# Performance work log

Hardware: AMD Instinct MI355X
Metric: run time of the kernel (lower is better)

## Reference

```python
import jax, jax.numpy as jnp
import numpy as np

NUM_UNITS = 64
NUM_NODES = 2048
COARSE_NODES = 256
INPUT_DIM = 1
BATCH = 64
AVG_DEGREE = 16


def _normalized_laplacian(adj):
    # A = A + I; L = D^-1/2 A^T D^-1/2 (matches scipy path in source)
    a = adj + np.eye(adj.shape[0], dtype=np.float64)
    d = a.sum(axis=1)
    d_inv_sqrt = np.power(d, -0.5)
    d_inv_sqrt[np.isinf(d_inv_sqrt)] = 0.0
    # (A @ D^-1/2).T @ D^-1/2 = A.T * d[:,None] * d[None,:]
    lap = a.T * d_inv_sqrt[:, None] * d_inv_sqrt[None, :]
    return lap.astype(np.float32)


def _random_adj(rng, n, deg):
    rows = np.repeat(np.arange(n), deg)
    cols = rng.integers(0, n, size=n * deg)
    a = np.zeros((n, n), dtype=np.float64)
    a[rows, cols] = 1.0
    a = np.maximum(a, a.T)  # symmetric
    np.fill_diagonal(a, 0.0)
    return a


def _xavier(key, shape):
    std = np.sqrt(2.0 / (shape[0] + shape[1]))
    return jax.random.normal(key, shape, dtype=jnp.float32) * std


def setup_inputs() -> dict:
    key = jax.random.key(0)
    ks = jax.random.split(key, 8)
    rng = np.random.default_rng(0)

    adj = jnp.asarray(_normalized_laplacian(_random_adj(rng, NUM_NODES, AVG_DEGREE)))
    adj1 = jnp.asarray(_normalized_laplacian(_random_adj(rng, COARSE_NODES, AVG_DEGREE)))
    # afc_mx in source is (num_nodes, coarse_nodes); afc = afc_mx.T, afct = afc_mx
    afc_mx = rng.random((NUM_NODES, COARSE_NODES)).astype(np.float32)
    afc = jnp.asarray(afc_mx.T)   # (C, N)
    afct = jnp.asarray(afc_mx)    # (N, C)

    in_size = INPUT_DIM + NUM_UNITS
    inputs = jax.random.normal(ks[0], (BATCH, NUM_NODES * INPUT_DIM), dtype=jnp.float32)
    state = jax.random.normal(ks[1], (BATCH, NUM_NODES * NUM_UNITS), dtype=jnp.float32)

    return {
        "inputs": inputs, "state": state,
        "adj": adj, "adj1": adj1, "afc": afc, "afct": afct,
        "w0": _xavier(ks[2], (in_size, 2 * NUM_UNITS)),
        "b0": jnp.zeros((2 * NUM_UNITS,), jnp.float32),
        "w1": _xavier(ks[3], (in_size, NUM_UNITS)),
        "b1": jnp.zeros((NUM_UNITS,), jnp.float32),
        "w01": _xavier(ks[4], (in_size, 2 * NUM_UNITS)),
        "b01": jnp.zeros((2 * NUM_UNITS,), jnp.float32),
        "w11": _xavier(ks[5], (in_size, NUM_UNITS)),
        "b11": jnp.zeros((NUM_UNITS,), jnp.float32),
    }


def _gc(inputs, state, adj, adj1, afc, afct, w, b, wf, bf):
    B = inputs.shape[0]
    N, C = adj.shape[0], adj1.shape[0]
    x = jnp.concatenate([inputs.reshape(B, N, -1), state.reshape(B, N, -1)], axis=2)
    F = x.shape[2]
    x0 = x.transpose(1, 2, 0).reshape(N, F * B)          # (N, F*B)
    x0fc = afc @ x0                                      # (C, F*B)
    x1 = adj @ x0                                        # graph conv, fine graph
    x1fc = adj1 @ x0fc                                   # graph conv, coarse graph
    x1 = x1 + jax.nn.sigmoid(afct @ x0fc)                # cross term fine<-coarse
    x1fc = x1fc + jax.nn.sigmoid(afc @ x1)               # cross term coarse<-fine
    out = x1.reshape(N, F, B).transpose(2, 0, 1).reshape(-1, F) @ w + b
    outfc = x1fc.reshape(C, F, B).transpose(2, 0, 1).reshape(-1, F) @ wf + bf
    return out.reshape(B, N, -1), outfc.reshape(B, C, -1)


def reference(inputs, state, adj, adj1, afc, afct, w0, b0, w1, b1, w01, b01, w11, b11):
    B = inputs.shape[0]
    N, U = NUM_NODES, NUM_UNITS
    x1, _x1fc = _gc(inputs, state, adj, adj1, afc, afct, w0, b0, w01, b01)
    value = jax.nn.sigmoid(x1)                           # (B, N, 2U)
    r, u = value[..., :U], value[..., U:]
    r = r.reshape(B, N * U)
    u = u.reshape(B, N * U)
    c0, _c1 = _gc(inputs, r * state, adj, adj1, afc, afct, w1, b1, w11, b11)
    c = jnp.tanh(c0).reshape(B, N * U)
    new_state = u * state + (1.0 - u) * c
    return new_state
```

## Files before the change

### kernel.cpp

```cpp
#include <hip/hip_runtime.h>
#include <hip/hip_bf16.h>
#include <math.h>

#define N_NODES 2048
#define C_NODES 256
#define BATCH   64
#define UNITS   64
#define JS      4096
#define NX      4160
#define JSX     4224
#define NU      131072
#define XSTR    4160
#define CAP     192

typedef short  s16x8 __attribute__((ext_vector_type(8)));
typedef float  f32x4 __attribute__((ext_vector_type(4)));

__device__ __forceinline__ float sigmoidf_(float x) { return 1.0f / (1.0f + __expf(-x)); }

__device__ __forceinline__ float bfs2f(short s) {
    union { float f; unsigned u; } w; w.u = ((unsigned)(unsigned short)s) << 16; return w.f;
}
__device__ __forceinline__ short f2bfs(float f) {
    __hip_bfloat16 h = __float2bfloat16(f);
    short s; __builtin_memcpy(&s, &h, 2); return s;
}

__device__ __forceinline__ void gload_lds16(const void* g, void* l) {
    __builtin_amdgcn_global_load_lds(
        (const __attribute__((address_space(1))) void*)g,
        (__attribute__((address_space(3))) void*)l, 16, 0, 0);
}

__global__ __launch_bounds__(256) void cvt_split(const float* __restrict__ s,
                                                 __hip_bfloat16* __restrict__ dh,
                                                 __hip_bfloat16* __restrict__ dl, int n)
{
    int stride = gridDim.x * 256;
    for (int i = blockIdx.x * 256 + threadIdx.x; i < n; i += stride) {
        float v = s[i];
        __hip_bfloat16 h = __float2bfloat16(v);
        dh[i] = h;
        dl[i] = __float2bfloat16(v - __bfloat162float(h));
    }
}

__global__ __launch_bounds__(256) void cvt_w(const float* __restrict__ w0,
                                             const float* __restrict__ w1,
                                             __hip_bfloat16* __restrict__ w0h, __hip_bfloat16* __restrict__ w0l,
                                             __hip_bfloat16* __restrict__ w1h, __hip_bfloat16* __restrict__ w1l)
{
    int stride = gridDim.x * 256;
    for (int e = blockIdx.x * 256 + threadIdx.x; e < 8192 + 4096; e += stride) {
        if (e < 8192) {
            int jj = e & 7, cell = e >> 3;
            int o = cell & 127, c = cell >> 7;
            float v = w0[(size_t)(1 + c * 8 + jj) * 128 + o];
            __hip_bfloat16 h = __float2bfloat16(v);
            w0h[e] = h; w0l[e] = __float2bfloat16(v - __bfloat162float(h));
        } else {
            int e2 = e - 8192;
            int jj = e2 & 7, cell = e2 >> 3;
            int o = cell & 63, c = cell >> 6;
            float v = w1[(size_t)(1 + c * 8 + jj) * 64 + o];
            __hip_bfloat16 h = __float2bfloat16(v);
            w1h[e2] = h; w1l[e2] = __float2bfloat16(v - __bfloat162float(h));
        }
    }
}

__global__ __launch_bounds__(256) void setup_ext(
    const float* __restrict__ inputs,
    __hip_bfloat16* __restrict__ xh, __hip_bfloat16* __restrict__ xl,
    __hip_bfloat16* __restrict__ fh, __hip_bfloat16* __restrict__ fl,
    __hip_bfloat16* __restrict__ X)
{
    int blk = blockIdx.x;
    if (blk < 64) {
        int b = blk;
        for (int n = threadIdx.x; n < N_NODES; n += 256) {
            float v = inputs[(size_t)b * N_NODES + n];
            __hip_bfloat16 h = __float2bfloat16(v);
            size_t o = (size_t)(JS + b) * N_NODES + n;
            xh[o] = h;
            xl[o] = __float2bfloat16(v - __bfloat162float(h));
            X[(size_t)n * XSTR + 4096 + b] = h;
        }
    } else {
        int r = NX + (blk - 64);
        __hip_bfloat16 z = __float2bfloat16(0.0f);
        for (int n = threadIdx.x; n < N_NODES; n += 256) {
            size_t o = (size_t)r * N_NODES + n;
            xh[o] = z; xl[o] = z;
        }
        for (int c = threadIdx.x; c < C_NODES; c += 256) {
            size_t o = (size_t)r * C_NODES + c;
            fh[o] = z; fl[o] = z;
        }
    }
}

__global__ __launch_bounds__(256) void build_csr(
    const float* __restrict__ adj,
    unsigned short* __restrict__ cols,
    float* __restrict__ vals,
    int* __restrict__ nnz)
{
    int row  = blockIdx.x * 4 + (threadIdx.x >> 6);
    int lane = threadIdx.x & 63;
    const float* a = adj + (size_t)row * N_NODES;
    int base = 0;
    for (int k0 = 0; k0 < N_NODES; k0 += 64) {
        float v = a[k0 + lane];
        unsigned long long m = __ballot(v != 0.0f);
        if (v != 0.0f) {
            int pos = base + __popcll(m & ((1ull << lane) - 1));
            if (pos < CAP) {
                cols[(size_t)row * CAP + pos] = (unsigned short)(k0 + lane);
                vals[(size_t)row * CAP + pos] = v;
            }
        }
        base += __popcll(m);
    }
    if (lane == 0) nnz[row] = base < CAP ? base : CAP;
}

__global__ __launch_bounds__(256) void build_x0sT(const float* __restrict__ st,
                                                  __hip_bfloat16* __restrict__ xh,
                                                  __hip_bfloat16* __restrict__ xl,
                                                  __hip_bfloat16* __restrict__ X)
{
    __shared__ float Ls[64 * 65];
    int n0 = blockIdx.x * 64;
    int b  = blockIdx.y;
    int t  = threadIdx.x;
    #pragma unroll
    for (int it = 0; it < 16; it++) {
        int idx = t + it * 256;
        int i = idx >> 6, u = idx & 63;
        float v = st[(size_t)b * NU + (size_t)(n0 + i) * 64 + u];
        Ls[i * 65 + u] = v;
        X[(size_t)(n0 + i) * XSTR + b * 64 + u] = __float2bfloat16(v);
    }
    __syncthreads();
    #pragma unroll
    for (int it = 0; it < 16; it++) {
        int idx = t + it * 256;
        int u = idx >> 6, i = idx & 63;
        float v = Ls[i * 65 + u];
        __hip_bfloat16 h = __float2bfloat16(v);
        size_t o = (size_t)(b * 64 + u) * N_NODES + n0 + i;
        xh[o] = h;
        xl[o] = __float2bfloat16(v - __bfloat162float(h));
    }
}

__global__ __launch_bounds__(256) void gemm1_split(
    const __hip_bfloat16* __restrict__ Ah, const __hip_bfloat16* __restrict__ Al,
    const __hip_bfloat16* __restrict__ Bh, const __hip_bfloat16* __restrict__ Bl,
    float* __restrict__ part)
{
    __shared__ __align__(16) __hip_bfloat16 AsH[4096];
    __shared__ __align__(16) __hip_bfloat16 AsL[4096];
    __shared__ __align__(16) __hip_bfloat16 BsH[4096];
    __shared__ __align__(16) __hip_bfloat16 BsL[4096];

    const int K = N_NODES;
    int tid  = threadIdx.x;
    int wave = tid >> 6, lane = tid & 63;
    int quad = lane >> 4, lr = lane & 15;
    int mBase = blockIdx.y * 64;
    int nBase = blockIdx.x * 64;
    int k0base = blockIdx.z * (K / 2);

    const __hip_bfloat16 *gAh[2], *gAl[2], *gBh[2], *gBl[2];
    __hip_bfloat16 *lAh[2], *lAl[2], *lBh[2], *lBl[2];
    #pragma unroll
    for (int ch = 0; ch < 2; ch++) {
        int cell = (wave * 2 + ch) * 64 + lane;
        int kb = cell >> 6, mm = cell & 63;
        size_t offA = (size_t)(mBase + mm) * K + k0base + kb * 8;
        size_t offB = (size_t)(nBase + mm) * K + k0base + kb * 8;
        gAh[ch] = Ah + offA; gAl[ch] = Al + offA;
        gBh[ch] = Bh + offB; gBl[ch] = Bl + offB;
        int lo = (wave * 2 + ch) * 512;
        lAh[ch] = AsH + lo; lAl[ch] = AsL + lo;
        lBh[ch] = BsH + lo; lBl[ch] = BsL + lo;
    }

    f32x4 acc[4];
    #pragma unroll
    for (int j = 0; j < 4; j++) { f32x4 z = {0.f,0.f,0.f,0.f}; acc[j] = z; }

    for (int k0 = 0; k0 < K / 2; k0 += 64) {
        #pragma unroll
        for (int ch = 0; ch < 2; ch++) {
            gload_lds16(gAh[ch] + k0, lAh[ch]);
            gload_lds16(gAl[ch] + k0, lAl[ch]);
            gload_lds16(gBh[ch] + k0, lBh[ch]);
            gload_lds16(gBl[ch] + k0, lBl[ch]);
        }
        __syncthreads();
        const s16x8* AhV = (const s16x8*)AsH;
        const s16x8* AlV = (const s16x8*)AsL;
        const s16x8* BhV = (const s16x8*)BsH;
        const s16x8* BlV = (const s16x8*)BsL;
        #pragma unroll
        for (int ks = 0; ks < 2; ks++) {
            int kb = ks * 4 + quad;
            s16x8 ah = AhV[kb * 64 + wave * 16 + lr];
            s16x8 al = AlV[kb * 64 + wave * 16 + lr];
            s16x8 bh[4], bl[4];
            #pragma unroll
            for (int j = 0; j < 4; j++) {
                bh[j] = BhV[kb * 64 + j * 16 + lr];
                bl[j] = BlV[kb * 64 + j * 16 + lr];
            }
            #pragma unroll
            for (int j = 0; j < 4; j++) {
                acc[j] = __builtin_amdgcn_mfma_f32_16x16x32_bf16(ah, bh[j], acc[j], 0, 0, 0);
                acc[j] = __builtin_amdgcn_mfma_f32_16x16x32_bf16(ah, bl[j], acc[j], 0, 0, 0);
                acc[j] = __builtin_amdgcn_mfma_f32_16x16x32_bf16(al, bh[j], acc[j], 0, 0, 0);
            }
        }
        __syncthreads();
    }

    float* dst = part + (size_t)blockIdx.z * NX * C_NODES;
    #pragma unroll
    for (int j = 0; j < 4; j++)
        #pragma unroll
        for (int r = 0; r < 4; r++) {
            int row = mBase + wave * 16 + quad * 4 + r;
            int col = nBase + j * 16 + lr;
            dst[(size_t)row * C_NODES + col] = acc[j][r];
        }
}

__global__ __launch_bounds__(256) void reduce_split(const float* __restrict__ part,
                                                    __hip_bfloat16* __restrict__ oh,
                                                    __hip_bfloat16* __restrict__ ol, int n)
{
    int stride = gridDim.x * 256;
    for (int i = blockIdx.x * 256 + threadIdx.x; i < n; i += stride) {
        float v = part[i] + part[(size_t)n + i];
        __hip_bfloat16 h = __float2bfloat16(v);
        oh[i] = h;
        ol[i] = __float2bfloat16(v - __bfloat162float(h));
    }
}

__global__ __launch_bounds__(256, 2) void gemm_coarse(
    const __hip_bfloat16* __restrict__ Ah, const __hip_bfloat16* __restrict__ Al,
    const __hip_bfloat16* __restrict__ Bh, const __hip_bfloat16* __restrict__ Bl,
    __hip_bfloat16* __restrict__ OutH, __hip_bfloat16* __restrict__ OutL)
{
    __shared__ __align__(16) __hip_bfloat16 S1[8192];
    __shared__ __align__(16) __hip_bfloat16 S2[8192];
    __shared__ __align__(16) __hip_bfloat16 S3[8192];
    __shared__ __align__(16) __hip_bfloat16 S4[8192];

    int tid  = threadIdx.x;
    int wave = tid >> 6, lane = tid & 63;
    int quad = lane >> 4, lr = lane & 15;
    int wr = wave >> 1, wc = wave & 1;
    int mBase = blockIdx.y * 128, nBase = blockIdx.x * 128;

    int cellkb[4], cellmm[4];
    #pragma unroll
    for (int ch = 0; ch < 4; ch++) {
        int cell = (wave * 4 + ch) * 64 + lane;
        cellkb[ch] = cell >> 7;
        cellmm[ch] = cell & 127;
    }

    f32x4 acc[4][4];
    #pragma unroll
    for (int i = 0; i < 4; i++)
        #pragma unroll
        for (int j = 0; j < 4; j++) { f32x4 z = {0.f,0.f,0.f,0.f}; acc[i][j] = z; }

    for (int k0 = 0; k0 < C_NODES; k0 += 64) {
        #pragma unroll
        for (int ch = 0; ch < 4; ch++) {
            size_t offA = (size_t)(mBase + cellmm[ch]) * C_NODES + k0 + cellkb[ch] * 8;
            size_t offB = (size_t)(nBase + cellmm[ch]) * C_NODES + k0 + cellkb[ch] * 8;
            int lo = (wave * 4 + ch) * 512;
            gload_lds16(Ah + offA, S1 + lo);
            gload_lds16(Al + offA, S2 + lo);
            gload_lds16(Bh + offB, S3 + lo);
            gload_lds16(Bl + offB, S4 + lo);
        }
        __syncthreads();
        const s16x8* AhV = (const s16x8*)S1;
        const s16x8* AlV = (const s16x8*)S2;
        const s16x8* BhV = (const s16x8*)S3;
        const s16x8* BlV = (const s16x8*)S4;
        #pragma unroll
        for (int ks = 0; ks < 2; ks++) {
            int kb = ks * 4 + quad;
            s16x8 ah[4], al[4], bh[4], bl[4];
            #pragma unroll
            for (int i = 0; i < 4; i++) {
                int idx = kb * 128 + wr * 64 + i * 16 + lr;
                ah[i] = AhV[idx]; al[i] = AlV[idx];
            }
            #pragma unroll
            for (int j = 0; j < 4; j++) {
                int idx = kb * 128 + wc * 64 + j * 16 + lr;
                bh[j] = BhV[idx]; bl[j] = BlV[idx];
            }
            #pragma unroll
            for (int i = 0; i < 4; i++)
                #pragma unroll
                for (int j = 0; j < 4; j++) {
                    acc[i][j] = __builtin_amdgcn_mfma_f32_16x16x32_bf16(ah[i], bh[j], acc[i][j], 0, 0, 0);
                    acc[i][j] = __builtin_amdgcn_mfma_f32_16x16x32_bf16(ah[i], bl[j], acc[i][j], 0, 0, 0);
                    acc[i][j] = __builtin_amdgcn_mfma_f32_16x16x32_bf16(al[i], bh[j], acc[i][j], 0, 0, 0);
                }
        }
        __syncthreads();
    }

    #pragma unroll
    for (int i = 0; i < 4; i++)
        #pragma unroll
        for (int j = 0; j < 4; j++)
            #pragma unroll
            for (int r = 0; r < 4; r++) {
                int row = mBase + wr * 64 + i * 16 + quad * 4 + r;
                int col = nBase + wc * 64 + j * 16 + lr;
                float v = sigmoidf_(acc[i][j][r]);
                size_t idx = (size_t)(col >> 6) * NU + (size_t)row * 64 + (col & 63);
                __hip_bfloat16 h = __float2bfloat16(v);
                OutH[idx] = h;
                OutL[idx] = __float2bfloat16(v - __bfloat162float(h));
            }
}

__global__ __launch_bounds__(256) void spmm_add(
    const __hip_bfloat16* __restrict__ X,
    const unsigned short* __restrict__ cols,
    const float* __restrict__ vals,
    const int* __restrict__ nnz,
    __hip_bfloat16* __restrict__ OutH,
    __hip_bfloat16* __restrict__ OutL)
{
    int wave = threadIdx.x >> 6, lane = threadIdx.x & 63;
    int n  = blockIdx.x * 4 + wave;
    int jt = blockIdx.y;
    int cnt = nnz[n];
    const unsigned short* cp = cols + (size_t)n * CAP;
    const float*          vp = vals + (size_t)n * CAP;
    const short* Xs = (const short*)X;

    if (jt < 8) {
        int j0 = jt * 512 + lane * 8;
        float acc[8];
        #pragma unroll
        for (int e = 0; e < 8; e++) acc[e] = 0.f;
        int i = 0;
        for (; i + 4 <= cnt; i += 4) {
            int   c0 = cp[i+0], c1 = cp[i+1], c2 = cp[i+2], c3 = cp[i+3];
            float a0 = vp[i+0], a1 = vp[i+1], a2 = vp[i+2], a3 = vp[i+3];
            s16x8 x0 = *(const s16x8*)(Xs + (size_t)c0 * XSTR + j0);
            s16x8 x1 = *(const s16x8*)(Xs + (size_t)c1 * XSTR + j0);
            s16x8 x2 = *(const s16x8*)(Xs + (size_t)c2 * XSTR + j0);
            s16x8 x3 = *(const s16x8*)(Xs + (size_t)c3 * XSTR + j0);
            #pragma unroll
            for (int e = 0; e < 8; e++)
                acc[e] += a0 * bfs2f(x0[e]) + a1 * bfs2f(x1[e])
                        + a2 * bfs2f(x2[e]) + a3 * bfs2f(x3[e]);
        }
        for (; i < cnt; i++) {
            int c = cp[i]; float a = vp[i];
            s16x8 xv = *(const s16x8*)(Xs + (size_t)c * XSTR + j0);
            #pragma unroll
            for (int e = 0; e < 8; e++) acc[e] += a * bfs2f(xv[e]);
        }
        size_t o = (size_t)(jt * 8 + (lane >> 3)) * NU + (size_t)n * 64 + (lane & 7) * 8;
        s16x8 h = *(const s16x8*)((const short*)OutH + o);
        s16x8 l = *(const s16x8*)((const short*)OutL + o);
        s16x8 nh, nl;
        #pragma unroll
        for (int e = 0; e < 8; e++) {
            float v = bfs2f(h[e]) + bfs2f(l[e]) + acc[e];
            short hh = f2bfs(v);
            nh[e] = hh;
            nl[e] = f2bfs(v - bfs2f(hh));
        }
        *(s16x8*)((short*)OutH + o) = nh;
        *(s16x8*)((short*)OutL + o) = nl;
    } else {
        float acc = 0.f;
        for (int i = 0; i < cnt; i++) {
            int c = cp[i]; float a = vp[i];
            acc += a * bfs2f(Xs[(size_t)c * XSTR + 4096 + lane]);
        }
        size_t o = (size_t)64 * NU + (size_t)n * 64 + lane;
        float v = bfs2f(((const short*)OutH)[o]) + bfs2f(((const short*)OutL)[o]) + acc;
        short hh = f2bfs(v);
        ((short*)OutH)[o] = hh;
        ((short*)OutL)[o] = f2bfs(v - bfs2f(hh));
    }
}

__global__ __launch_bounds__(256, 4) void head1_mfma(
    const __hip_bfloat16* __restrict__ x1h, const __hip_bfloat16* __restrict__ x1l,
    const __hip_bfloat16* __restrict__ Wh, const __hip_bfloat16* __restrict__ Wl,
    const float* __restrict__ w0, const float* __restrict__ b0,
    const float* __restrict__ state,
    __hip_bfloat16* __restrict__ xh, __hip_bfloat16* __restrict__ xl,
    __hip_bfloat16* __restrict__ u_buf,
    __hip_bfloat16* __restrict__ Xout)
{
    __shared__ __align__(16) short trH[8192];
    __shared__ __align__(16) short trL[8192];
    __shared__ float xinS[128];

    int n0 = blockIdx.x * 128;
    int b  = blockIdx.y;
    int tid = threadIdx.x;
    int wave = tid >> 6, lane = tid & 63;
    int quad = lane >> 4, lr = lane & 15;
    int wr = wave >> 1, wc = wave & 1;

    if (tid < 128) {
        size_t o = (size_t)64 * NU + (size_t)(n0 + tid) * 64 + b;
        xinS[tid] = __bfloat162float(x1h[o]) + __bfloat162float(x1l[o]);
    }

    f32x4 acc[4][4];
    #pragma unroll
    for (int i = 0; i < 4; i++)
        #pragma unroll
        for (int j = 0; j < 4; j++) { f32x4 z = {0.f,0.f,0.f,0.f}; acc[i][j] = z; }

    const short* Xh = (const short*)x1h + (size_t)b * NU;
    const short* Xl = (const short*)x1l + (size_t)b * NU;
    const short* Wh_ = (const short*)Wh;
    const short* Wl_ = (const short*)Wl;

    #pragma unroll
    for (int ks = 0; ks < 2; ks++) {
        s16x8 ah[4], al[4];
        #pragma unroll
        for (int i = 0; i < 4; i++) {
            size_t off = (size_t)(n0 + wr * 64 + i * 16 + lr) * 64 + ks * 32 + quad * 8;
            ah[i] = *(const s16x8*)(Xh + off);
            al[i] = *(const s16x8*)(Xl + off);
        }
        #pragma unroll
        for (int j = 0; j < 4; j++) {
            size_t wo = ((size_t)(ks * 4 + quad) * 128 + wc * 64 + j * 16 + lr) * 8;
            s16x8 bh = *(const s16x8*)(Wh_ + wo);
            s16x8 bl = *(const s16x8*)(Wl_ + wo);
            #pragma unroll
            for (int i = 0; i < 4; i++) {
                acc[i][j] = __builtin_amdgcn_mfma_f32_16x16x32_bf16(ah[i], bh, acc[i][j], 0, 0, 0);
                acc[i][j] = __builtin_amdgcn_mfma_f32_16x16x32_bf16(ah[i], bl, acc[i][j], 0, 0, 0);
                acc[i][j] = __builtin_amdgcn_mfma_f32_16x16x32_bf16(al[i], bh, acc[i][j], 0, 0, 0);
            }
        }
    }
    __syncthreads();

    #pragma unroll
    for (int i = 0; i < 4; i++)
        #pragma unroll
        for (int j = 0; j < 4; j++)
            #pragma unroll
            for (int r = 0; r < 4; r++) {
                int n_loc = wr * 64 + i * 16 + quad * 4 + r;
                int o = wc * 64 + j * 16 + lr;
                float g = acc[i][j][r] + w0[o] * xinS[n_loc] + b0[o];
                float sg = sigmoidf_(g);
                if (wc == 0) {
                    float sv = state[(size_t)b * NU + (size_t)(n0 + n_loc) * 64 + o];
                    float rs = sg * sv;
                    short h = f2bfs(rs);
                    int sw = n_loc ^ ((o & 15) << 3);
                    trH[o * 128 + sw] = h;
                    trL[o * 128 + sw] = f2bfs(rs - bfs2f(h));
                    ((short*)Xout)[(size_t)(n0 + n_loc) * XSTR + b * 64 + o] = h;
                } else {
                    u_buf[(size_t)b * NU + (size_t)(n0 + n_loc) * 64 + (o - 64)] = __float2bfloat16(sg);
                }
            }
    __syncthreads();

    {
        int row = tid >> 2, seg = tid & 3;
        int xorv = (row & 15) << 3;
        short* dh = (short*)xh + (size_t)(b * 64 + row) * N_NODES + n0 + seg * 32;
        short* dl = (short*)xl + (size_t)(b * 64 + row) * N_NODES + n0 + seg * 32;
        #pragma unroll
        for (int q = 0; q < 4; q++) {
            int src = row * 128 + ((seg * 32 + q * 8) ^ xorv);
            *(uint4*)(dh + q * 8) = *(const uint4*)(trH + src);
            *(uint4*)(dl + q * 8) = *(const uint4*)(trL + src);
        }
    }
}

__global__ __launch_bounds__(256, 4) void head2_mfma(
    const __hip_bfloat16* __restrict__ x1h, const __hip_bfloat16* __restrict__ x1l,
    const __hip_bfloat16* __restrict__ Wh, const __hip_bfloat16* __restrict__ Wl,
    const float* __restrict__ w1, const float* __restrict__ b1,
    const float* __restrict__ state, const __hip_bfloat16* __restrict__ u_buf,
    float* __restrict__ out)
{
    __shared__ float xinS[128];

    int n0 = blockIdx.x * 128;
    int b  = blockIdx.y;
    int tid = threadIdx.x;
    int wave = tid >> 6, lane = tid & 63;
    int quad = lane >> 4, lr = lane & 15;

    if (tid < 128) {
        size_t o = (size_t)64 * NU + (size_t)(n0 + tid) * 64 + b;
        xinS[tid] = __bfloat162float(x1h[o]) + __bfloat162float(x1l[o]);
    }

    f32x4 acc[2][4];
    #pragma unroll
    for (int i = 0; i < 2; i++)
        #pragma unroll
        for (int j = 0; j < 4; j++) { f32x4 z = {0.f,0.f,0.f,0.f}; acc[i][j] = z; }

    const short* Xh = (const short*)x1h + (size_t)b * NU;
    const short* Xl = (const short*)x1l + (size_t)b * NU;
    const short* Wh_ = (const short*)Wh;
    const short* Wl_ = (const short*)Wl;

    #pragma unroll
    for (int ks = 0; ks < 2; ks++) {
        s16x8 ah[2], al[2];
        #pragma unroll
        for (int i = 0; i < 2; i++) {
            size_t off = (size_t)(n0 + wave * 32 + i * 16 + lr) * 64 + ks * 32 + quad * 8;
            ah[i] = *(const s16x8*)(Xh + off);
            al[i] = *(const s16x8*)(Xl + off);
        }
        #pragma unroll
        for (int j = 0; j < 4; j++) {
            size_t wo = ((size_t)(ks * 4 + quad) * 64 + j * 16 + lr) * 8;
            s16x8 bh = *(const s16x8*)(Wh_ + wo);
            s16x8 bl = *(const s16x8*)(Wl_ + wo);
            #pragma unroll
            for (int i = 0; i < 2; i++) {
                acc[i][j] = __builtin_amdgcn_mfma_f32_16x16x32_bf16(ah[i], bh, acc[i][j], 0, 0, 0);
                acc[i][j] = __builtin_amdgcn_mfma_f32_16x16x32_bf16(ah[i], bl, acc[i][j], 0, 0, 0);
                acc[i][j] = __builtin_amdgcn_mfma_f32_16x16x32_bf16(al[i], bh, acc[i][j], 0, 0, 0);
            }
        }
    }
    __syncthreads();

    #pragma unroll
    for (int i = 0; i < 2; i++)
        #pragma unroll
        for (int j = 0; j < 4; j++)
            #pragma unroll
            for (int r = 0; r < 4; r++) {
                int n_loc = wave * 32 + i * 16 + quad * 4 + r;
                int o = j * 16 + lr;
                float g = acc[i][j][r] + w1[o] * xinS[n_loc] + b1[o];
                float c = tanhf(g);
                size_t sidx = (size_t)b * NU + (size_t)(n0 + n_loc) * 64 + o;
                float ug = __bfloat162float(u_buf[sidx]);
                float sv = state[sidx];
                out[sidx] = ug * sv + (1.0f - ug) * c;
            }
}

extern "C" void kernel_launch(void* const* d_in, const int* in_sizes, int n_in,
                              void* d_out, int out_size, void* d_ws, size_t ws_size,
                              hipStream_t stream)
{
    const float* inputs = (const float*)d_in[0];
    const float* state  = (const float*)d_in[1];
    const float* adj    = (const float*)d_in[2];
    const float* afc    = (const float*)d_in[4];
    const float* afct   = (const float*)d_in[5];
    const float* w0     = (const float*)d_in[6];
    const float* b0     = (const float*)d_in[7];
    const float* w1     = (const float*)d_in[8];
    const float* b1     = (const float*)d_in[9];

    float* out = (float*)d_out;

    char* p = (char*)d_ws;
    __hip_bfloat16* afc_h    = (__hip_bfloat16*)p; p += (size_t)C_NODES * N_NODES * 2;
    __hip_bfloat16* afc_l    = (__hip_bfloat16*)p; p += (size_t)C_NODES * N_NODES * 2;
    __hip_bfloat16* afct_h   = (__hip_bfloat16*)p; p += (size_t)N_NODES * C_NODES * 2;
    __hip_bfloat16* afct_l   = (__hip_bfloat16*)p; p += (size_t)N_NODES * C_NODES * 2;
    __hip_bfloat16* w0T_h    = (__hip_bfloat16*)p; p += 8192 * 2;
    __hip_bfloat16* w0T_l    = (__hip_bfloat16*)p; p += 8192 * 2;
    __hip_bfloat16* w1T_h    = (__hip_bfloat16*)p; p += 4096 * 2;
    __hip_bfloat16* w1T_l    = (__hip_bfloat16*)p; p += 4096 * 2;
    __hip_bfloat16* x0sT_h   = (__hip_bfloat16*)p; p += (size_t)JSX * N_NODES * 2;
    __hip_bfloat16* x0sT_l   = (__hip_bfloat16*)p; p += (size_t)JSX * N_NODES * 2;
    __hip_bfloat16* x0fcT_h  = (__hip_bfloat16*)p; p += (size_t)JSX * C_NODES * 2;
    __hip_bfloat16* x0fcT_l  = (__hip_bfloat16*)p; p += (size_t)JSX * C_NODES * 2;
    __hip_bfloat16* x1B_h    = (__hip_bfloat16*)p; p += (size_t)66 * NU * 2;
    __hip_bfloat16* x1B_l    = (__hip_bfloat16*)p; p += (size_t)66 * NU * 2;
    __hip_bfloat16* u_buf    = (__hip_bfloat16*)p; p += (size_t)BATCH * NU * 2;
    float*          part     = (float*)p;          p += (size_t)2 * NX * C_NODES * 4;
    __hip_bfloat16* X        = (__hip_bfloat16*)p; p += (size_t)N_NODES * XSTR * 2;
    unsigned short* csr_cols = (unsigned short*)p; p += (size_t)N_NODES * CAP * 2;
    float*          csr_vals = (float*)p;          p += (size_t)N_NODES * CAP * 4;
    int*            csr_nnz  = (int*)p;            p += (size_t)N_NODES * 4;

    dim3 blk(256);

    cvt_split<<<256,  blk, 0, stream>>>(afc,  afc_h,  afc_l,  C_NODES * N_NODES);
    cvt_split<<<256,  blk, 0, stream>>>(afct, afct_h, afct_l, N_NODES * C_NODES);
    cvt_w    <<<32,   blk, 0, stream>>>(w0, w1, w0T_h, w0T_l, w1T_h, w1T_l);
    setup_ext<<<128,  blk, 0, stream>>>(inputs, x0sT_h, x0sT_l, x0fcT_h, x0fcT_l, X);
    build_csr<<<512,  blk, 0, stream>>>(adj, csr_cols, csr_vals, csr_nnz);

    build_x0sT<<<dim3(32, 64), blk, 0, stream>>>(state, x0sT_h, x0sT_l, X);
    gemm1_split<<<dim3(4, 65, 2), blk, 0, stream>>>(x0sT_h, x0sT_l, afc_h, afc_l, part);
    reduce_split<<<1024, blk, 0, stream>>>(part, x0fcT_h, x0fcT_l, NX * C_NODES);
    gemm_coarse<<<dim3(33, 16), blk, 0, stream>>>(afct_h, afct_l, x0fcT_h, x0fcT_l, x1B_h, x1B_l);
    spmm_add<<<dim3(512, 9), blk, 0, stream>>>(X, csr_cols, csr_vals, csr_nnz, x1B_h, x1B_l);
    head1_mfma<<<dim3(16, 64), blk, 0, stream>>>(x1B_h, x1B_l, w0T_h, w0T_l, w0, b0,
                                                 state, x0sT_h, x0sT_l, u_buf, X);

    gemm1_split<<<dim3(4, 65, 2), blk, 0, stream>>>(x0sT_h, x0sT_l, afc_h, afc_l, part);
    reduce_split<<<1024, blk, 0, stream>>>(part, x0fcT_h, x0fcT_l, NX * C_NODES);
    gemm_coarse<<<dim3(33, 16), blk, 0, stream>>>(afct_h, afct_l, x0fcT_h, x0fcT_l, x1B_h, x1B_l);
    spmm_add<<<dim3(512, 9), blk, 0, stream>>>(X, csr_cols, csr_vals, csr_nnz, x1B_h, x1B_l);
    head2_mfma<<<dim3(16, 64), blk, 0, stream>>>(x1B_h, x1B_l, w1T_h, w1T_l, w1, b1,
                                                 state, u_buf, out);
}
```

Baseline: 529.9 us.

## Use 128x128 tiles with 8-way split-K for afc GEMM and alias partials

Replaces the 64x64, 2-way split-K GEMM computing afc @ x0 with a 128x128-tile, 8-way split-K kernel. A is staged in LDS and B is read directly from global memory into registers. The reduce kernel now sums 8 partial slices. The partial buffer is aliased onto the x1B buffers, which are dead at that point, to save workspace. More tile reuse and more blocks come at the cost of four times more partial-sum traffic in the reduction.

```diff
diff --git a/kernel.cpp b/kernel.cpp
--- a/kernel.cpp
+++ b/kernel.cpp
@@ -12,6 +12,7 @@
 #define NU      131072
 #define XSTR    4160
 #define CAP     192
+#define ZSPLIT  8
 
 typedef short  s16x8 __attribute__((ext_vector_type(8)));
 typedef float  f32x4 __attribute__((ext_vector_type(4)));
@@ -155,86 +156,87 @@
     }
 }
 
-__global__ __launch_bounds__(256) void gemm1_split(
+__global__ __launch_bounds__(256) void gemm1_mfma128(
     const __hip_bfloat16* __restrict__ Ah, const __hip_bfloat16* __restrict__ Al,
     const __hip_bfloat16* __restrict__ Bh, const __hip_bfloat16* __restrict__ Bl,
     float* __restrict__ part)
 {
-    __shared__ __align__(16) __hip_bfloat16 AsH[4096];
-    __shared__ __align__(16) __hip_bfloat16 AsL[4096];
-    __shared__ __align__(16) __hip_bfloat16 BsH[4096];
-    __shared__ __align__(16) __hip_bfloat16 BsL[4096];
+    __shared__ __align__(16) __hip_bfloat16 S1[8192];
+    __shared__ __align__(16) __hip_bfloat16 S2[8192];
 
     const int K = N_NODES;
     int tid  = threadIdx.x;
     int wave = tid >> 6, lane = tid & 63;
     int quad = lane >> 4, lr = lane & 15;
-    int mBase = blockIdx.y * 64;
-    int nBase = blockIdx.x * 64;
-    int k0base = blockIdx.z * (K / 2);
-
-    const __hip_bfloat16 *gAh[2], *gAl[2], *gBh[2], *gBl[2];
-    __hip_bfloat16 *lAh[2], *lAl[2], *lBh[2], *lBl[2];
-    #pragma unroll
-    for (int ch = 0; ch < 2; ch++) {
-        int cell = (wave * 2 + ch) * 64 + lane;
-        int kb = cell >> 6, mm = cell & 63;
-        size_t offA = (size_t)(mBase + mm) * K + k0base + kb * 8;
-        size_t offB = (size_t)(nBase + mm) * K + k0base + kb * 8;
-        gAh[ch] = Ah + offA; gAl[ch] = Al + offA;
-        gBh[ch] = Bh + offB; gBl[ch] = Bl + offB;
-        int lo = (wave * 2 + ch) * 512;
-        lAh[ch] = AsH + lo; lAl[ch] = AsL + lo;
-        lBh[ch] = BsH + lo; lBl[ch] = BsL + lo;
-    }
-
-    f32x4 acc[4];
-    #pragma unroll
-    for (int j = 0; j < 4; j++) { f32x4 z = {0.f,0.f,0.f,0.f}; acc[j] = z; }
-
-    for (int k0 = 0; k0 < K / 2; k0 += 64) {
-        #pragma unroll
-        for (int ch = 0; ch < 2; ch++) {
-            gload_lds16(gAh[ch] + k0, lAh[ch]);
-            gload_lds16(gAl[ch] + k0, lAl[ch]);
-            gload_lds16(gBh[ch] + k0, lBh[ch]);
-            gload_lds16(gBl[ch] + k0, lBl[ch]);
+    int wr = wave >> 1, wc = wave & 1;
+    int mBase = blockIdx.y * 128;
+    int nBase = blockIdx.x * 128;
+    int k0base = blockIdx.z * (K / ZSPLIT);
+
+    int cellkb[4], cellmm[4];
+    #pragma unroll
+    for (int ch = 0; ch < 4; ch++) {
+        int cell = (wave * 4 + ch) * 64 + lane;
+        cellkb[ch] = cell >> 7;
+        cellmm[ch] = cell & 127;
+    }
+
+    f32x4 acc[4][4];
+    #pragma unroll
+    for (int i = 0; i < 4; i++)
+        #pragma unroll
+        for (int j = 0; j < 4; j++) { f32x4 z = {0.f,0.f,0.f,0.f}; acc[i][j] = z; }
+
+    const short* Bh_ = (const short*)Bh;
+    const short* Bl_ = (const short*)Bl;
+
+    for (int k0 = 0; k0 < K / ZSPLIT; k0 += 64) {
+        #pragma unroll
+        for (int ch = 0; ch < 4; ch++) {
+            size_t offA = (size_t)(mBase + cellmm[ch]) * K + k0base + k0 + cellkb[ch] * 8;
+            int lo = (wave * 4 + ch) * 512;
+            gload_lds16(Ah + offA, S1 + lo);
+            gload_lds16(Al + offA, S2 + lo);
         }
         __syncthreads();
-        const s16x8* AhV = (const s16x8*)AsH;
-        const s16x8* AlV = (const s16x8*)AsL;
-        const s16x8* BhV = (const s16x8*)BsH;
-        const s16x8* BlV = (const s16x8*)BsL;
+        const s16x8* AhV = (const s16x8*)S1;
+        const s16x8* AlV = (const s16x8*)S2;
         #pragma unroll
         for (int ks = 0; ks < 2; ks++) {
             int kb = ks * 4 + quad;
-            s16x8 ah = AhV[kb * 64 + wave * 16 + lr];
-            s16x8 al = AlV[kb * 64 + wave * 16 + lr];
-            s16x8 bh[4], bl[4];
+            s16x8 ah[4], al[4];
+            #pragma unroll
+            for (int i = 0; i < 4; i++) {
+                int idx = kb * 128 + wr * 64 + i * 16 + lr;
+                ah[i] = AhV[idx]; al[i] = AlV[idx];
+            }
             #pragma unroll
             for (int j = 0; j < 4; j++) {
-                bh[j] = BhV[kb * 64 + j * 16 + lr];
-                bl[j] = BlV[kb * 64 + j * 16 + lr];
-            }
-            #pragma unroll
-            for (int j = 0; j < 4; j++) {
-                acc[j] = __builtin_amdgcn_mfma_f32_16x16x32_bf16(ah, bh[j], acc[j], 0, 0, 0);
-                acc[j] = __builtin_amdgcn_mfma_f32_16x16x32_bf16(ah, bl[j], acc[j], 0, 0, 0);
-                acc[j] = __builtin_amdgcn_mfma_f32_16x16x32_bf16(al, bh[j], acc[j], 0, 0, 0);
+                size_t bo = (size_t)(nBase + wc * 64 + j * 16 + lr) * K + k0base + k0 + kb * 8;
+                s16x8 bh = *(const s16x8*)(Bh_ + bo);
+                s16x8 bl = *(const s16x8*)(Bl_ + bo);
+                #pragma unroll
+                for (int i = 0; i < 4; i++) {
+                    acc[i][j] = __builtin_amdgcn_mfma_f32_16x16x32_bf16(ah[i], bh, acc[i][j], 0, 0, 0);
+                    acc[i][j] = __builtin_amdgcn_mfma_f32_16x16x32_bf16(ah[i], bl, acc[i][j], 0, 0, 0);
+                    acc[i][j] = __builtin_amdgcn_mfma_f32_16x16x32_bf16(al[i], bh, acc[i][j], 0, 0, 0);
+                }
             }
         }
         __syncthreads();
     }
 
-    float* dst = part + (size_t)blockIdx.z * NX * C_NODES;
-    #pragma unroll
-    for (int j = 0; j < 4; j++)
-        #pragma unroll
-        for (int r = 0; r < 4; r++) {
-            int row = mBase + wave * 16 + quad * 4 + r;
-            int col = nBase + j * 16 + lr;
-            dst[(size_t)row * C_NODES + col] = acc[j][r];
-        }
+    float* dst = part + (size_t)blockIdx.z * JSX * C_NODES;
+    #pragma unroll
+    for (int i = 0; i < 4; i++)
+        #pragma unroll
+        for (int j = 0; j < 4; j++)
+            #pragma unroll
+            for (int r = 0; r < 4; r++) {
+                int row = mBase + wr * 64 + i * 16 + quad * 4 + r;
+                int col = nBase + wc * 64 + j * 16 + lr;
+                dst[(size_t)row * C_NODES + col] = acc[i][j][r];
+            }
 }
 
 __global__ __launch_bounds__(256) void reduce_split(const float* __restrict__ part,
@@ -242,8 +244,11 @@
                                                     __hip_bfloat16* __restrict__ ol, int n)
 {
     int stride = gridDim.x * 256;
+    const size_t slice = (size_t)JSX * C_NODES;
     for (int i = blockIdx.x * 256 + threadIdx.x; i < n; i += stride) {
-        float v = part[i] + part[(size_t)n + i];
+        float v = 0.f;
+        #pragma unroll
+        for (int s = 0; s < ZSPLIT; s++) v += part[s * slice + i];
         __hip_bfloat16 h = __float2bfloat16(v);
         oh[i] = h;
         ol[i] = __float2bfloat16(v - __bfloat162float(h));
@@ -604,10 +609,10 @@
     __hip_bfloat16* x0sT_l   = (__hip_bfloat16*)p; p += (size_t)JSX * N_NODES * 2;
     __hip_bfloat16* x0fcT_h  = (__hip_bfloat16*)p; p += (size_t)JSX * C_NODES * 2;
     __hip_bfloat16* x0fcT_l  = (__hip_bfloat16*)p; p += (size_t)JSX * C_NODES * 2;
+    float*          part     = (float*)p;
     __hip_bfloat16* x1B_h    = (__hip_bfloat16*)p; p += (size_t)66 * NU * 2;
     __hip_bfloat16* x1B_l    = (__hip_bfloat16*)p; p += (size_t)66 * NU * 2;
     __hip_bfloat16* u_buf    = (__hip_bfloat16*)p; p += (size_t)BATCH * NU * 2;
-    float*          part     = (float*)p;          p += (size_t)2 * NX * C_NODES * 4;
     __hip_bfloat16* X        = (__hip_bfloat16*)p; p += (size_t)N_NODES * XSTR * 2;
     unsigned short* csr_cols = (unsigned short*)p; p += (size_t)N_NODES * CAP * 2;
     float*          csr_vals = (float*)p;          p += (size_t)N_NODES * CAP * 4;
@@ -622,14 +627,14 @@
     build_csr<<<512,  blk, 0, stream>>>(adj, csr_cols, csr_vals, csr_nnz);
 
     build_x0sT<<<dim3(32, 64), blk, 0, stream>>>(state, x0sT_h, x0sT_l, X);
-    gemm1_split<<<dim3(4, 65, 2), blk, 0, stream>>>(x0sT_h, x0sT_l, afc_h, afc_l, part);
+    gemm1_mfma128<<<dim3(2, 33, ZSPLIT), blk, 0, stream>>>(x0sT_h, x0sT_l, afc_h, afc_l, part);
     reduce_split<<<1024, blk, 0, stream>>>(part, x0fcT_h, x0fcT_l, NX * C_NODES);
     gemm_coarse<<<dim3(33, 16), blk, 0, stream>>>(afct_h, afct_l, x0fcT_h, x0fcT_l, x1B_h, x1B_l);
     spmm_add<<<dim3(512, 9), blk, 0, stream>>>(X, csr_cols, csr_vals, csr_nnz, x1B_h, x1B_l);
     head1_mfma<<<dim3(16, 64), blk, 0, stream>>>(x1B_h, x1B_l, w0T_h, w0T_l, w0, b0,
                                                  state, x0sT_h, x0sT_l, u_buf, X);
 
-    gemm1_split<<<dim3(4, 65, 2), blk, 0, stream>>>(x0sT_h, x0sT_l, afc_h, afc_l, part);
+    gemm1_mfma128<<<dim3(2, 33, ZSPLIT), blk, 0, stream>>>(x0sT_h, x0sT_l, afc_h, afc_l, part);
     reduce_split<<<1024, blk, 0, stream>>>(part, x0fcT_h, x0fcT_l, NX * C_NODES);
     gemm_coarse<<<dim3(33, 16), blk, 0, stream>>>(afct_h, afct_l, x0fcT_h, x0fcT_l, x1B_h, x1B_l);
     spmm_add<<<dim3(512, 9), blk, 0, stream>>>(X, csr_cols, csr_vals, csr_nnz, x1B_h, x1B_l);
```

Measured after the change: 515.7 us. 2.7% less time.
